# Optimization experiments

Hardware: AMD Instinct MI355X
Metric: run time of the kernel (lower is better)

The kernel has to match this reference:

```python
import jax, jax.numpy as jnp
import numpy as np

B, S, D = 2, 2048, 2048
H = 16
Q_LORA, KV_LORA = 1536, 512
ROPE_DIM, NOPE_DIM, V_DIM = 64, 64, 128
Q_HEAD_DIM = NOPE_DIM + ROPE_DIM  # 128
ROPE_THETA, ROPE_RATIO = 10000.0, 1.0


def setup_inputs() -> dict:
    key = jax.random.key(0)
    ks = jax.random.split(key, 6)
    std = 0.02
    return {
        "hidden_states": jax.random.normal(ks[0], (B, S, D), jnp.float32),
        "Wqa": jax.random.normal(ks[1], (D, Q_LORA), jnp.float32) * std,
        "Wqb": jax.random.normal(ks[2], (Q_LORA, H * Q_HEAD_DIM), jnp.float32) * std,
        "Wkva": jax.random.normal(ks[3], (D, KV_LORA + ROPE_DIM), jnp.float32) * std,
        "Wkvb": jax.random.normal(ks[4], (KV_LORA, H * (NOPE_DIM + V_DIM)), jnp.float32) * std,
        "Wo": jax.random.normal(ks[5], (H * V_DIM, D), jnp.float32) * std,
    }


def _rope_tables(seq_len):
    half = ROPE_DIM // 2
    inv_freq = ROPE_RATIO / (ROPE_THETA ** (jnp.arange(half, dtype=jnp.float32) * 2.0 / ROPE_DIM))
    freqs = jnp.arange(seq_len, dtype=jnp.float32)[:, None] * inv_freq[None, :]  # [S, half]
    return jnp.cos(freqs), jnp.sin(freqs)


def _apply_rope(x, cos, sin):
    # interleaved even/odd rotation, matches torch stack+flatten
    x_even = x[..., 0::2]
    x_odd = x[..., 1::2]
    r_even = x_even * cos - x_odd * sin
    r_odd = x_odd * cos + x_even * sin
    return jnp.stack([r_even, r_odd], axis=-1).reshape(x.shape)


def reference(hidden_states, Wqa, Wqb, Wkva, Wkvb, Wo):
    b, s, _ = hidden_states.shape
    scale = Q_HEAD_DIM ** -0.5

    # query compression path
    q_latent = hidden_states @ Wqa                             # [B,S,Q_LORA]
    q = (q_latent @ Wqb).reshape(b, s, H, Q_HEAD_DIM)
    q = jnp.transpose(q, (0, 2, 1, 3))                          # [B,H,S,q_head_dim]
    q_nope, q_pe = q[..., :NOPE_DIM], q[..., NOPE_DIM:]

    # kv compression
    kv_comp = hidden_states @ Wkva                              # [B,S,KV_LORA+ROPE]
    c_kv, k_pe = kv_comp[..., :KV_LORA], kv_comp[..., KV_LORA:]

    cos, sin = _rope_tables(s)                                  # [S, ROPE_DIM//2]
    q_pe = _apply_rope(q_pe, cos, sin)                          # [B,H,S,ROPE]
    k_pe = _apply_rope(k_pe, cos, sin)                          # [B,S,ROPE]

    # kv decompression
    kv = (c_kv @ Wkvb).reshape(b, s, H, NOPE_DIM + V_DIM)
    kv = jnp.transpose(kv, (0, 2, 1, 3))                        # [B,H,S,nope+v]
    k_nope, v = kv[..., :NOPE_DIM], kv[..., NOPE_DIM:]

    k_pe_b = jnp.broadcast_to(k_pe[:, None], (b, H, s, ROPE_DIM))
    q_full = jnp.concatenate([q_nope, q_pe], axis=-1)           # [B,H,S,128]
    k_full = jnp.concatenate([k_nope, k_pe_b], axis=-1)         # [B,H,S,128]

    scores = jnp.einsum('bhqd,bhkd->bhqk', q_full, k_full) * scale
    causal = jnp.tril(jnp.ones((s, s), dtype=bool))
    scores = jnp.where(causal[None, None], scores, jnp.finfo(scores.dtype).min)
    probs = jax.nn.softmax(scores, axis=-1)
    attn = jnp.einsum('bhqk,bhkd->bhqd', probs, v)              # [B,H,S,V_DIM]

    out = jnp.transpose(attn, (0, 2, 1, 3)).reshape(b, s, H * V_DIM)
    return out @ Wo                                             # [B,S,D]
```

## Files before the change

kernel.cpp:

```cpp
#include <hip/hip_runtime.h>
#include <hip/hip_bf16.h>
#include <cstdint>
#include <cstddef>

typedef __bf16 bf16_t;
typedef __attribute__((ext_vector_type(4))) __bf16 bf16x4;
typedef __attribute__((ext_vector_type(8))) __bf16 bf16x8;
typedef __attribute__((ext_vector_type(4))) float f32x4;

#define S_ 2048
#define H_ 16
#define NTOK 4096

__device__ __forceinline__ f32x4 mfma16x16(bf16x8 a, bf16x8 b, f32x4 c) {
  return __builtin_amdgcn_mfma_f32_16x16x32_bf16(a, b, c, 0, 0, 0);
}
__device__ __forceinline__ bf16x8 load8(const bf16_t* p) {
  return *reinterpret_cast<const bf16x8*>(p);
}
__device__ __forceinline__ void load_lds16(const void* g, void* l) {
  __builtin_amdgcn_global_load_lds(
      (const __attribute__((address_space(1))) uint32_t*)g,
      (__attribute__((address_space(3))) uint32_t*)l, 16, 0, 0);
}


__global__ void cast_bf16_k(const float* __restrict__ in, bf16_t* __restrict__ out, int n) {
  int idx = blockIdx.x * 256 + threadIdx.x;
  int i4 = idx * 4;
  if (i4 >= n) return;
  float4 v = *reinterpret_cast<const float4*>(in + i4);
  out[i4 + 0] = (bf16_t)v.x;
  out[i4 + 1] = (bf16_t)v.y;
  out[i4 + 2] = (bf16_t)v.z;
  out[i4 + 3] = (bf16_t)v.w;
}

__global__ void rope_tables_k(float* __restrict__ cosT, float* __restrict__ sinT) {
  int idx = blockIdx.x * 256 + threadIdx.x;
  if (idx >= S_ * 32) return;
  int s = idx >> 5, i = idx & 31;
  float inv = powf(10000.0f, -(2.0f * (float)i) / 64.0f);
  float fr = (float)s * inv;
  cosT[idx] = cosf(fr);
  sinT[idx] = sinf(fr);
}

struct TDesc {
  const float* src;
  bf16_t* dst;
  int K, Nsrc, bxc, off, perm;
};
struct TDesc5 {
  TDesc d[5];
};

__global__ void transpose_cast_multi_k(TDesc5 ds) {
  __shared__ float tile[32][33];
  const int bid = blockIdx.x;
  int i = 0;
#pragma unroll
  for (int j = 1; j < 5; ++j)
    if (bid >= ds.d[j].off) i = j;
  const float* __restrict__ in = ds.d[i].src;
  bf16_t* __restrict__ out = ds.d[i].dst;
  const int K = ds.d[i].K, Nsrc = ds.d[i].Nsrc;
  const int local = bid - ds.d[i].off;
  const int n0 = (local % ds.d[i].bxc) * 32;
  const int k0 = (local / ds.d[i].bxc) * 32;
  int srcn0 = n0;
  if (ds.d[i].perm) {
    srcn0 = (n0 < 1024) ? ((n0 >> 6) * 192 + (n0 & 63))
                        : (((n0 - 1024) >> 7) * 192 + 64 + ((n0 - 1024) & 127));
  }
  int tx = threadIdx.x & 31, ty = threadIdx.x >> 5;
#pragma unroll
  for (int r = 0; r < 4; ++r) {
    int k = k0 + ty + r * 8, n = srcn0 + tx;
    tile[ty + r * 8][tx] = (n < Nsrc) ? in[(size_t)k * Nsrc + n] : 0.0f;
  }
  __syncthreads();
#pragma unroll
  for (int r = 0; r < 4; ++r) {
    int n = n0 + ty + r * 8, k = k0 + tx;
    out[(size_t)n * K + k] = (bf16_t)tile[tx][ty + r * 8];
  }
}


__device__ __forceinline__ void gemm_loop64(const bf16_t* __restrict__ A, int lda,
                                            const bf16_t* __restrict__ Bt, int K, int m0, int n0,
                                            int tid, bf16_t* Al, bf16_t* Bl, f32x4 (&acc)[4][4]) {
  const int wid = tid >> 6, lane = tid & 63;
  const int wm = (wid >> 1) * 64, wn = (wid & 1) * 64;
  const int srow8 = lane >> 3, c8 = lane & 7;
  const int swz8 = c8 ^ srow8;
  const int lr = lane & 15, lg = lane >> 4;
  const int e = lr & 7;

  const bf16_t* ag = A + (size_t)(m0 + wid * 32 + srow8) * lda + (swz8 << 3);
  const bf16_t* bg = Bt + (size_t)(n0 + wid * 32 + srow8) * K + (swz8 << 3);

  auto STAGE = [&](int buf, int k0) {
    bf16_t* ab = Al + buf * (128 * 64);
    bf16_t* bb = Bl + buf * (128 * 64);
#pragma unroll
    for (int rr = 0; rr < 4; ++rr) {
      load_lds16(ag + (size_t)(rr * 8) * lda + k0, &ab[(wid * 32 + rr * 8) * 64]);
      load_lds16(bg + (size_t)(rr * 8) * K + k0, &bb[(wid * 32 + rr * 8) * 64]);
    }
  };

  STAGE(0, 0);
  int cur = 0;
  for (int k0 = 0; k0 < K; k0 += 64) {
    if (k0 + 64 < K) {
      STAGE(cur ^ 1, k0 + 64);
      __builtin_amdgcn_sched_barrier(0);
      asm volatile("s_waitcnt vmcnt(8)" ::: "memory");
    } else {
      asm volatile("s_waitcnt vmcnt(0)" ::: "memory");
    }
    __builtin_amdgcn_sched_barrier(0);
    __builtin_amdgcn_s_barrier();
    __builtin_amdgcn_sched_barrier(0);
    const bf16_t* Ab = Al + cur * (128 * 64);
    const bf16_t* Bb = Bl + cur * (128 * 64);
#pragma unroll
    for (int kk = 0; kk < 2; ++kk) {
      bf16x8 af[4], bfr[4];
#pragma unroll
      for (int i = 0; i < 4; ++i) {
        af[i] = load8(&Ab[(wm + i * 16 + lr) * 64 + (((kk * 4 + lg) ^ e) << 3)]);
        bfr[i] = load8(&Bb[(wn + i * 16 + lr) * 64 + (((kk * 4 + lg) ^ e) << 3)]);
      }
#pragma unroll
      for (int i = 0; i < 4; ++i)
#pragma unroll
        for (int j = 0; j < 4; ++j) acc[i][j] = mfma16x16(af[i], bfr[j], acc[i][j]);
    }
    __builtin_amdgcn_sched_barrier(0);
    __builtin_amdgcn_s_barrier();
    cur ^= 1;
  }
}


__global__ __launch_bounds__(256) void gemm_lat_k(const bf16_t* __restrict__ A,
                                                  const bf16_t* __restrict__ Bt,
                                                  bf16_t* __restrict__ C,
                                                  const float* __restrict__ cosT,
                                                  const float* __restrict__ sinT) {
  __shared__ alignas(16) bf16_t Al[2 * 128 * 64];
  __shared__ alignas(16) bf16_t Bl[2 * 128 * 64];
  const int tid = threadIdx.x;
  const int sw = (blockIdx.x & 7) * 68 + (blockIdx.x >> 3);
  const int m0 = (sw / 17) * 128, n0 = (sw % 17) * 128;
  f32x4 acc[4][4] = {};
  gemm_loop64(A, 2048, Bt, 2048, m0, n0, tid, Al, Bl, acc);

  const int wid = tid >> 6, lane = tid & 63;
  const int wm = (wid >> 1) * 64, wn = (wid & 1) * 64;
  const int lr = lane & 15, lg = lane >> 4;
  const bool rope = (n0 == 2048) && (wn == 0);
  const int ir_base = lr >> 1;
  const bool odd = lane & 1;
#pragma unroll
  for (int i = 0; i < 4; ++i)
#pragma unroll
    for (int j = 0; j < 4; ++j) {
      float v4[4];
#pragma unroll
      for (int r = 0; r < 4; ++r) v4[r] = acc[i][j][r];
      if (rope) {
        const int ir = j * 8 + ir_base;
#pragma unroll
        for (int r = 0; r < 4; ++r) {
          const int srow_ = (m0 + wm + i * 16 + lg * 4 + r) & (S_ - 1);
          float c = cosT[srow_ * 32 + ir], sn = sinT[srow_ * 32 + ir];
          float partner = __shfl_xor(v4[r], 1);
          v4[r] = odd ? (v4[r] * c + partner * sn) : (v4[r] * c - partner * sn);
        }
      }
#pragma unroll
      for (int r = 0; r < 4; ++r) {
        int row = m0 + wm + i * 16 + lg * 4 + r;
        int col = n0 + wn + j * 16 + lr;
        C[(size_t)row * 2176 + col] = (bf16_t)v4[r];
      }
    }
}


__global__ __launch_bounds__(256) void gemm_qkv_k(const bf16_t* __restrict__ lat,
                                                  const bf16_t* __restrict__ Wqbt,
                                                  const bf16_t* __restrict__ Wkvbt,
                                                  bf16_t* __restrict__ qb,
                                                  bf16_t* __restrict__ knb,
                                                  bf16_t* __restrict__ vT,
                                                  const float* __restrict__ cosT,
                                                  const float* __restrict__ sinT, float qscale) {
  __shared__ alignas(16) bf16_t Al[2 * 128 * 64];
  __shared__ alignas(16) bf16_t Bl[2 * 128 * 64];
  const int tid = threadIdx.x;
  const int sw = (blockIdx.x & 7) * 160 + (blockIdx.x >> 3);
  const int wid = tid >> 6, lane = tid & 63;
  const int wm = (wid >> 1) * 64, wn = (wid & 1) * 64;
  const int lr = lane & 15, lg = lane >> 4;
  f32x4 acc[4][4] = {};
  const int r5 = sw % 5, q5 = sw / 5;

  if (r5 < 2) {
    const int qi = q5 * 2 + r5;
    const int m0 = (qi >> 4) * 128, n0 = (qi & 15) * 128;
    gemm_loop64(lat, 2176, Wqbt, 1536, m0, n0, tid, Al, Bl, acc);
    const bool rope = (wn == 64);
    const int ir_base = lr >> 1;
    const bool odd = lane & 1;
#pragma unroll
    for (int i = 0; i < 4; ++i)
#pragma unroll
      for (int j = 0; j < 4; ++j) {
        float v4[4];
#pragma unroll
        for (int r = 0; r < 4; ++r) v4[r] = acc[i][j][r] * qscale;
        if (rope) {
          const int ir = j * 8 + ir_base;
#pragma unroll
          for (int r = 0; r < 4; ++r) {
            const int srow_ = (m0 + wm + i * 16 + lg * 4 + r) & (S_ - 1);
            float c = cosT[srow_ * 32 + ir], sn = sinT[srow_ * 32 + ir];
            float partner = __shfl_xor(v4[r], 1);
            v4[r] = odd ? (v4[r] * c + partner * sn) : (v4[r] * c - partner * sn);
          }
        }
#pragma unroll
        for (int r = 0; r < 4; ++r) {
          int row = m0 + wm + i * 16 + lg * 4 + r;
          int col = n0 + wn + j * 16 + lr;
          qb[(size_t)row * 2048 + col] = (bf16_t)v4[r];
        }
      }
  } else {
    const int ki = q5 * 3 + (r5 - 2);
    const int m0 = (ki / 24) * 128, n0 = (ki % 24) * 128;
    gemm_loop64(lat + 1536, 2176, Wkvbt, 512, m0, n0, tid, Al, Bl, acc);
    if (n0 < 1024) {
#pragma unroll
      for (int i = 0; i < 4; ++i)
#pragma unroll
        for (int j = 0; j < 4; ++j)
#pragma unroll
          for (int r = 0; r < 4; ++r) {
            int row = m0 + wm + i * 16 + lg * 4 + r;
            int col = n0 + wn + j * 16 + lr;
            knb[(size_t)row * 1024 + col] = (bf16_t)acc[i][j][r];
          }
    } else {
#pragma unroll
      for (int i = 0; i < 4; ++i) {
        const int row0 = m0 + wm + i * 16 + lg * 4;
        const int bb = row0 >> 11;
        const int s0 = row0 & (S_ - 1);
#pragma unroll
        for (int j = 0; j < 4; ++j) {
          const int idx = n0 + wn + j * 16 + lr - 1024;
          const int h = idx >> 7, d = idx & 127;
          bf16x4 pk;
#pragma unroll
          for (int r = 0; r < 4; ++r) pk[r] = (bf16_t)acc[i][j][r];
          *reinterpret_cast<bf16x4*>(&vT[((size_t)(bb * 16 + h) * 128 + d) * 2048 + s0]) = pk;
        }
      }
    }
  }
}


__global__ __launch_bounds__(256) void gemm_out_k(const bf16_t* __restrict__ A,
                                                  const bf16_t* __restrict__ Bt,
                                                  float* __restrict__ C) {
  __shared__ alignas(16) bf16_t Al[2 * 128 * 64];
  __shared__ alignas(16) bf16_t Bl[2 * 128 * 64];
  const int tid = threadIdx.x;
  const int sw = (blockIdx.x & 7) * 64 + (blockIdx.x >> 3);
  const int m0 = (sw >> 4) * 128, n0 = (sw & 15) * 128;
  f32x4 acc[4][4] = {};
  gemm_loop64(A, 2048, Bt, 2048, m0, n0, tid, Al, Bl, acc);
  const int wid = tid >> 6, lane = tid & 63;
  const int wm = (wid >> 1) * 64, wn = (wid & 1) * 64;
  const int lr = lane & 15, lg = lane >> 4;
#pragma unroll
  for (int i = 0; i < 4; ++i)
#pragma unroll
    for (int j = 0; j < 4; ++j)
#pragma unroll
      for (int r = 0; r < 4; ++r) {
        int row = m0 + wm + i * 16 + lg * 4 + r;
        int col = n0 + wn + j * 16 + lr;
        C[(size_t)row * 2048 + col] = acc[i][j][r];
      }
}

__global__ __launch_bounds__(256) void attn_fused(const bf16_t* __restrict__ q,
                                                  const bf16_t* __restrict__ knb,
                                                  const bf16_t* __restrict__ lat,
                                                  const bf16_t* __restrict__ vT,
                                                  bf16_t* __restrict__ out) {
  __shared__ alignas(16) bf16_t Kn[64 * 64];
  __shared__ alignas(16) bf16_t Kp[64 * 64];
  __shared__ alignas(16) bf16_t Vt[128 * 64];
  __shared__ alignas(16) bf16_t Pl[4][16 * 64];
  const int tid = threadIdx.x, wid = tid >> 6, lane = tid & 63;
  const int bid = blockIdx.x;
  const int g = bid >> 8;
  const int x = (bid >> 5) & 7;
  const int bh = bid & 31;
  const int qt = (g & 1) ? (24 - g * 8 + x) : (31 - g * 8 - x);
  const int b = bh >> 4, h = bh & 15;
  const int tokb = b * S_;
  const int lr = lane & 15, lg = lane >> 4;
  const int srow8 = lane >> 3, c8 = lane & 7;
  const int swz8 = c8 ^ srow8;
  bf16_t* Pw = &Pl[wid][0];

  bf16x8 ones;
#pragma unroll
  for (int j = 0; j < 8; ++j) ones[j] = (bf16_t)1.0f;

  bf16x8 qf[4];
  {
    const int qrow = qt * 64 + wid * 16 + lr;
    const bf16_t* qp = q + (size_t)(tokb + qrow) * 2048 + h * 128 + lg * 8;
#pragma unroll
    for (int ds = 0; ds < 4; ++ds) qf[ds] = load8(qp + ds * 32);
  }

  f32x4 o[8] = {};
  f32x4 o8 = {};
  float m = -1e30f;
  const int qr_glob = qt * 64 + wid * 16 + lr;

  for (int t = 0; t <= qt; ++t) {
    const int kb = t * 64;
#pragma unroll
    for (int rr = 0; rr < 2; ++rr) {
      const int r0 = wid * 16 + rr * 8;
      const size_t tk = (size_t)(tokb + kb + r0 + srow8);
      load_lds16(knb + tk * 1024 + h * 64 + (swz8 << 3), &Kn[r0 * 64]);
      load_lds16(lat + tk * 2176 + 2048 + (swz8 << 3), &Kp[r0 * 64]);
    }
#pragma unroll
    for (int rr = 0; rr < 4; ++rr) {
      const int r0 = wid * 32 + rr * 8;
      load_lds16(vT + ((size_t)bh * 128 + r0 + srow8) * 2048 + kb + (swz8 << 3), &Vt[r0 * 64]);
    }
    __syncthreads();

    f32x4 s[4];
    __builtin_amdgcn_s_setprio(1);
#pragma unroll
    for (int kt = 0; kt < 4; ++kt) {
      const int row = kt * 16 + lr;
      const int e = lr & 7;
      bf16x8 kf0 = load8(&Kn[row * 64 + ((lg ^ e) << 3)]);
      bf16x8 kf1 = load8(&Kn[row * 64 + (((lg + 4) ^ e) << 3)]);
      bf16x8 kf2 = load8(&Kp[row * 64 + ((lg ^ e) << 3)]);
      bf16x8 kf3 = load8(&Kp[row * 64 + (((lg + 4) ^ e) << 3)]);
      f32x4 acc = {0.f, 0.f, 0.f, 0.f};
      acc = mfma16x16(kf0, qf[0], acc);
      acc = mfma16x16(kf1, qf[1], acc);
      acc = mfma16x16(kf2, qf[2], acc);
      acc = mfma16x16(kf3, qf[3], acc);
      s[kt] = acc;
    }
    __builtin_amdgcn_s_setprio(0);

    if (t == qt) {
#pragma unroll
      for (int kt = 0; kt < 4; ++kt)
#pragma unroll
        for (int r = 0; r < 4; ++r) {
          const int key = kb + kt * 16 + lg * 4 + r;
          if (key > qr_glob) s[kt][r] = -1e30f;
        }
    }

    float tm;
    {
      float a0 = fmaxf(fmaxf(s[0][0], s[0][1]), fmaxf(s[0][2], s[0][3]));
      float a1 = fmaxf(fmaxf(s[1][0], s[1][1]), fmaxf(s[1][2], s[1][3]));
      float a2 = fmaxf(fmaxf(s[2][0], s[2][1]), fmaxf(s[2][2], s[2][3]));
      float a3 = fmaxf(fmaxf(s[3][0], s[3][1]), fmaxf(s[3][2], s[3][3]));
      tm = fmaxf(fmaxf(a0, a1), fmaxf(a2, a3));
      tm = fmaxf(tm, __shfl_xor(tm, 16));
      tm = fmaxf(tm, __shfl_xor(tm, 32));
    }
    if (!__all(tm - m <= 8.0f)) {
      float mn = fmaxf(m, tm);
      float corr = exp2f(m - mn);
      m = mn;
      float corrv[4];
#pragma unroll
      for (int r = 0; r < 4; ++r) corrv[r] = __shfl(corr, lg * 4 + r);
#pragma unroll
      for (int r = 0; r < 4; ++r) {
        o8[r] *= corrv[r];
#pragma unroll
        for (int n = 0; n < 8; ++n) o[n][r] *= corrv[r];
      }
    }
#pragma unroll
    for (int kt = 0; kt < 4; ++kt)
#pragma unroll
      for (int r = 0; r < 4; ++r) s[kt][r] = exp2f(s[kt][r] - m);

#pragma unroll
    for (int kt = 0; kt < 4; ++kt) {
      bf16x4 pk;
#pragma unroll
      for (int r = 0; r < 4; ++r) pk[r] = (bf16_t)s[kt][r];
      const int c = kt * 2 + (lg >> 1);
      *reinterpret_cast<bf16x4*>(&Pw[lr * 64 + ((c ^ (lr & 7)) << 3) + ((lg & 1) << 2)]) = pk;
    }

    __builtin_amdgcn_s_setprio(1);
#pragma unroll
    for (int ks = 0; ks < 2; ++ks) {
      const int e = lr & 7;
      bf16x8 pa = load8(&Pw[lr * 64 + (((ks * 4 + lg) ^ e) << 3)]);
#pragma unroll
      for (int n = 0; n < 8; ++n) {
        bf16x8 vb = load8(&Vt[(n * 16 + lr) * 64 + (((ks * 4 + lg) ^ e) << 3)]);
        o[n] = mfma16x16(pa, vb, o[n]);
      }
      o8 = mfma16x16(pa, ones, o8);
    }
    __builtin_amdgcn_s_setprio(0);
    __syncthreads();
  }

  float linv[4];
#pragma unroll
  for (int r = 0; r < 4; ++r) linv[r] = __builtin_amdgcn_rcpf(o8[r]);
#pragma unroll
  for (int n = 0; n < 8; ++n)
#pragma unroll
    for (int r = 0; r < 4; ++r) {
      const int qr = qt * 64 + wid * 16 + lg * 4 + r;
      out[(size_t)(tokb + qr) * 2048 + h * 128 + n * 16 + lr] = (bf16_t)(o[n][r] * linv[r]);
    }
}


extern "C" void kernel_launch(void* const* d_in, const int* in_sizes, int n_in, void* d_out,
                              int out_size, void* d_ws, size_t ws_size, hipStream_t stream) {
  const float* hs = (const float*)d_in[0];
  const float* Wqa = (const float*)d_in[1];
  const float* Wqb = (const float*)d_in[2];
  const float* Wkva = (const float*)d_in[3];
  const float* Wkvb = (const float*)d_in[4];
  const float* Wo = (const float*)d_in[5];
  float* out = (float*)d_out;

  char* ws = (char*)d_ws;
  size_t off = 0;
  auto alloc = [&](size_t bytes) {
    void* p = ws + off;
    off += (bytes + 255) & ~(size_t)255;
    return p;
  };
  bf16_t* hsb = (bf16_t*)alloc((size_t)NTOK * 2048 * 2);
  bf16_t* W1t = (bf16_t*)alloc((size_t)2176 * 2048 * 2);
  bf16_t* Wqbt = (bf16_t*)alloc((size_t)2048 * 1536 * 2);
  bf16_t* Wkvbt = (bf16_t*)alloc((size_t)3072 * 512 * 2);
  bf16_t* Wot = (bf16_t*)alloc((size_t)2048 * 2048 * 2);
  bf16_t* lat = (bf16_t*)alloc((size_t)NTOK * 2176 * 2);
  bf16_t* qb = (bf16_t*)alloc((size_t)NTOK * 2048 * 2);
  bf16_t* knb = (bf16_t*)alloc((size_t)NTOK * 1024 * 2);
  bf16_t* attn = (bf16_t*)alloc((size_t)NTOK * 2048 * 2);
  bf16_t* vT = (bf16_t*)alloc((size_t)32 * 128 * 2048 * 2);
  float* cosT = (float*)alloc((size_t)S_ * 32 * 4);
  float* sinT = (float*)alloc((size_t)S_ * 32 * 4);

  cast_bf16_k<<<(NTOK * 2048 / 4 + 255) / 256, 256, 0, stream>>>(hs, hsb, NTOK * 2048);
  rope_tables_k<<<(S_ * 32 + 255) / 256, 256, 0, stream>>>(cosT, sinT);
  {
    TDesc5 ds;
    int o0 = 0;
    auto add = [&](int i, const float* src, bf16_t* dst, int K, int Nsrc, int Nout, int perm) {
      int bxc = Nout / 32, cnt = bxc * (K / 32);
      ds.d[i] = TDesc{src, dst, K, Nsrc, bxc, o0, perm};
      o0 += cnt;
    };
    add(0, Wqa, W1t, 2048, 1536, 1536, 0);
    add(1, Wkva, W1t + (size_t)1536 * 2048, 2048, 576, 640, 0);
    add(2, Wqb, Wqbt, 1536, 2048, 2048, 0);
    add(3, Wkvb, Wkvbt, 512, 3072, 3072, 1);
    add(4, Wo, Wot, 2048, 2048, 2048, 0);
    transpose_cast_multi_k<<<o0, 256, 0, stream>>>(ds);
  }

  gemm_lat_k<<<dim3(544), 256, 0, stream>>>(hsb, W1t, lat, cosT, sinT);
  const float scale = 0.08838834764831845f * 1.4426950408889634f;
  gemm_qkv_k<<<dim3(1280), 256, 0, stream>>>(lat, Wqbt, Wkvbt, qb, knb, vT, cosT, sinT, scale);
  attn_fused<<<dim3(1024), 256, 0, stream>>>(qb, knb, lat, vT, attn);
  gemm_out_k<<<dim3(512), 256, 0, stream>>>(attn, Wot, out);
}
```

Baseline: 275.3 us.

## Double-buffer K/V tiles in attention to overlap global-to-LDS loads with compute

Splits the K-nope, K-rope and V-transpose LDS tiles into two buffers and issues the load of tile t+1 before computing on tile t. A manual vmcnt wait and s_barrier replace the per-iteration __syncthreads so the prefetch stays in flight during the MFMA work. LDS use rises from about 40 KB to 72 KB per block, which may lower occupancy, and the hand-written waitcnt count has to match the number of loads issued per stage.

```diff
diff --git a/kernel.cpp b/kernel.cpp
--- a/kernel.cpp
+++ b/kernel.cpp
@@ -307,9 +307,9 @@
                                                   const bf16_t* __restrict__ lat,
                                                   const bf16_t* __restrict__ vT,
                                                   bf16_t* __restrict__ out) {
-  __shared__ alignas(16) bf16_t Kn[64 * 64];
-  __shared__ alignas(16) bf16_t Kp[64 * 64];
-  __shared__ alignas(16) bf16_t Vt[128 * 64];
+  __shared__ alignas(16) bf16_t Kn[2][64 * 64];
+  __shared__ alignas(16) bf16_t Kp[2][64 * 64];
+  __shared__ alignas(16) bf16_t Vt[2][128 * 64];
   __shared__ alignas(16) bf16_t Pl[4][16 * 64];
   const int tid = threadIdx.x, wid = tid >> 6, lane = tid & 63;
   const int bid = blockIdx.x;
@@ -341,21 +341,36 @@
   float m = -1e30f;
   const int qr_glob = qt * 64 + wid * 16 + lr;
 
-  for (int t = 0; t <= qt; ++t) {
+  auto STAGE = [&](int buf, int t) {
     const int kb = t * 64;
 #pragma unroll
     for (int rr = 0; rr < 2; ++rr) {
       const int r0 = wid * 16 + rr * 8;
       const size_t tk = (size_t)(tokb + kb + r0 + srow8);
-      load_lds16(knb + tk * 1024 + h * 64 + (swz8 << 3), &Kn[r0 * 64]);
-      load_lds16(lat + tk * 2176 + 2048 + (swz8 << 3), &Kp[r0 * 64]);
+      load_lds16(knb + tk * 1024 + h * 64 + (swz8 << 3), &Kn[buf][r0 * 64]);
+      load_lds16(lat + tk * 2176 + 2048 + (swz8 << 3), &Kp[buf][r0 * 64]);
     }
 #pragma unroll
     for (int rr = 0; rr < 4; ++rr) {
       const int r0 = wid * 32 + rr * 8;
-      load_lds16(vT + ((size_t)bh * 128 + r0 + srow8) * 2048 + kb + (swz8 << 3), &Vt[r0 * 64]);
-    }
-    __syncthreads();
+      load_lds16(vT + ((size_t)bh * 128 + r0 + srow8) * 2048 + kb + (swz8 << 3),
+                 &Vt[buf][r0 * 64]);
+    }
+  };
+
+  STAGE(0, 0);
+  for (int t = 0; t <= qt; ++t) {
+    const int cur = t & 1;
+    if (t < qt) {
+      STAGE(cur ^ 1, t + 1);
+      __builtin_amdgcn_sched_barrier(0);
+      asm volatile("s_waitcnt vmcnt(8)" ::: "memory");
+    } else {
+      asm volatile("s_waitcnt vmcnt(0)" ::: "memory");
+    }
+    __builtin_amdgcn_sched_barrier(0);
+    __builtin_amdgcn_s_barrier();
+    __builtin_amdgcn_sched_barrier(0);
 
     f32x4 s[4];
     __builtin_amdgcn_s_setprio(1);
@@ -363,10 +378,10 @@
     for (int kt = 0; kt < 4; ++kt) {
       const int row = kt * 16 + lr;
       const int e = lr & 7;
-      bf16x8 kf0 = load8(&Kn[row * 64 + ((lg ^ e) << 3)]);
-      bf16x8 kf1 = load8(&Kn[row * 64 + (((lg + 4) ^ e) << 3)]);
-      bf16x8 kf2 = load8(&Kp[row * 64 + ((lg ^ e) << 3)]);
-      bf16x8 kf3 = load8(&Kp[row * 64 + (((lg + 4) ^ e) << 3)]);
+      bf16x8 kf0 = load8(&Kn[cur][row * 64 + ((lg ^ e) << 3)]);
+      bf16x8 kf1 = load8(&Kn[cur][row * 64 + (((lg + 4) ^ e) << 3)]);
+      bf16x8 kf2 = load8(&Kp[cur][row * 64 + ((lg ^ e) << 3)]);
+      bf16x8 kf3 = load8(&Kp[cur][row * 64 + (((lg + 4) ^ e) << 3)]);
       f32x4 acc = {0.f, 0.f, 0.f, 0.f};
       acc = mfma16x16(kf0, qf[0], acc);
       acc = mfma16x16(kf1, qf[1], acc);
@@ -377,6 +392,7 @@
     __builtin_amdgcn_s_setprio(0);
 
     if (t == qt) {
+      const int kb = t * 64;
 #pragma unroll
       for (int kt = 0; kt < 4; ++kt)
 #pragma unroll
@@ -431,13 +447,14 @@
       bf16x8 pa = load8(&Pw[lr * 64 + (((ks * 4 + lg) ^ e) << 3)]);
 #pragma unroll
       for (int n = 0; n < 8; ++n) {
-        bf16x8 vb = load8(&Vt[(n * 16 + lr) * 64 + (((ks * 4 + lg) ^ e) << 3)]);
+        bf16x8 vb = load8(&Vt[cur][(n * 16 + lr) * 64 + (((ks * 4 + lg) ^ e) << 3)]);
         o[n] = mfma16x16(pa, vb, o[n]);
       }
       o8 = mfma16x16(pa, ones, o8);
     }
     __builtin_amdgcn_s_setprio(0);
-    __syncthreads();
+    __builtin_amdgcn_sched_barrier(0);
+    __builtin_amdgcn_s_barrier();
   }
 
   float linv[4];
```

Result: no change. 277.2 us (+0.7%).

## Switch attention to 32x32x16 MFMA with two waves per block

Applied to the files above, without the earlier changes.

Rewrites the fused attention kernel to use 32x32x16 bf16 MFMA instructions, with each of two waves handling 32 query rows instead of four waves with 16 rows each. Blocks shrink to 128 threads and each wave loads more of the K/V tiles into LDS. The goal is better MFMA efficiency and fewer LDS fragment reads per FLOP. In exchange, per-wave register pressure rises from the larger accumulators, and there are fewer waves per block to hide latency.

```diff
diff --git a/kernel.cpp b/kernel.cpp
--- a/kernel.cpp
+++ b/kernel.cpp
@@ -7,6 +7,7 @@
 typedef __attribute__((ext_vector_type(4))) __bf16 bf16x4;
 typedef __attribute__((ext_vector_type(8))) __bf16 bf16x8;
 typedef __attribute__((ext_vector_type(4))) float f32x4;
+typedef __attribute__((ext_vector_type(16))) float f32x16;
 
 #define S_ 2048
 #define H_ 16
@@ -14,6 +15,9 @@
 
 __device__ __forceinline__ f32x4 mfma16x16(bf16x8 a, bf16x8 b, f32x4 c) {
   return __builtin_amdgcn_mfma_f32_16x16x32_bf16(a, b, c, 0, 0, 0);
+}
+__device__ __forceinline__ f32x16 mfma32(bf16x8 a, bf16x8 b, f32x16 c) {
+  return __builtin_amdgcn_mfma_f32_32x32x16_bf16(a, b, c, 0, 0, 0);
 }
 __device__ __forceinline__ bf16x8 load8(const bf16_t* p) {
   return *reinterpret_cast<const bf16x8*>(p);
@@ -302,7 +306,7 @@
       }
 }
 
-__global__ __launch_bounds__(256) void attn_fused(const bf16_t* __restrict__ q,
+__global__ __launch_bounds__(128) void attn_fused(const bf16_t* __restrict__ q,
                                                   const bf16_t* __restrict__ knb,
                                                   const bf16_t* __restrict__ lat,
                                                   const bf16_t* __restrict__ vT,
@@ -310,8 +314,8 @@
   __shared__ alignas(16) bf16_t Kn[64 * 64];
   __shared__ alignas(16) bf16_t Kp[64 * 64];
   __shared__ alignas(16) bf16_t Vt[128 * 64];
-  __shared__ alignas(16) bf16_t Pl[4][16 * 64];
-  const int tid = threadIdx.x, wid = tid >> 6, lane = tid & 63;
+  __shared__ alignas(16) bf16_t Pl[2][32 * 64];
+  const int tid = threadIdx.x, wv = tid >> 6, lane = tid & 63;
   const int bid = blockIdx.x;
   const int g = bid >> 8;
   const int x = (bid >> 5) & 7;
@@ -319,136 +323,135 @@
   const int qt = (g & 1) ? (24 - g * 8 + x) : (31 - g * 8 - x);
   const int b = bh >> 4, h = bh & 15;
   const int tokb = b * S_;
-  const int lr = lane & 15, lg = lane >> 4;
+  const int l31 = lane & 31, hi = lane >> 5;
+  const int e7 = l31 & 7;
   const int srow8 = lane >> 3, c8 = lane & 7;
   const int swz8 = c8 ^ srow8;
-  bf16_t* Pw = &Pl[wid][0];
+  bf16_t* Pw = &Pl[wv][0];
 
   bf16x8 ones;
 #pragma unroll
   for (int j = 0; j < 8; ++j) ones[j] = (bf16_t)1.0f;
 
-  bf16x8 qf[4];
+  const int qrow = qt * 64 + wv * 32 + l31;
+  bf16x8 qf[8];
   {
-    const int qrow = qt * 64 + wid * 16 + lr;
-    const bf16_t* qp = q + (size_t)(tokb + qrow) * 2048 + h * 128 + lg * 8;
-#pragma unroll
-    for (int ds = 0; ds < 4; ++ds) qf[ds] = load8(qp + ds * 32);
-  }
-
-  f32x4 o[8] = {};
-  f32x4 o8 = {};
+    const bf16_t* qp = q + (size_t)(tokb + qrow) * 2048 + h * 128 + hi * 8;
+#pragma unroll
+    for (int grp = 0; grp < 8; ++grp) qf[grp] = load8(qp + grp * 16);
+  }
+
+  f32x16 o[4] = {};
+  f32x16 o8 = {};
   float m = -1e30f;
-  const int qr_glob = qt * 64 + wid * 16 + lr;
 
   for (int t = 0; t <= qt; ++t) {
     const int kb = t * 64;
 #pragma unroll
-    for (int rr = 0; rr < 2; ++rr) {
-      const int r0 = wid * 16 + rr * 8;
+    for (int rr = 0; rr < 4; ++rr) {
+      const int r0 = wv * 32 + rr * 8;
       const size_t tk = (size_t)(tokb + kb + r0 + srow8);
       load_lds16(knb + tk * 1024 + h * 64 + (swz8 << 3), &Kn[r0 * 64]);
       load_lds16(lat + tk * 2176 + 2048 + (swz8 << 3), &Kp[r0 * 64]);
     }
 #pragma unroll
-    for (int rr = 0; rr < 4; ++rr) {
-      const int r0 = wid * 32 + rr * 8;
+    for (int rr = 0; rr < 8; ++rr) {
+      const int r0 = wv * 64 + rr * 8;
       load_lds16(vT + ((size_t)bh * 128 + r0 + srow8) * 2048 + kb + (swz8 << 3), &Vt[r0 * 64]);
     }
     __syncthreads();
 
-    f32x4 s[4];
+    f32x16 sv[2];
     __builtin_amdgcn_s_setprio(1);
 #pragma unroll
-    for (int kt = 0; kt < 4; ++kt) {
-      const int row = kt * 16 + lr;
-      const int e = lr & 7;
-      bf16x8 kf0 = load8(&Kn[row * 64 + ((lg ^ e) << 3)]);
-      bf16x8 kf1 = load8(&Kn[row * 64 + (((lg + 4) ^ e) << 3)]);
-      bf16x8 kf2 = load8(&Kp[row * 64 + ((lg ^ e) << 3)]);
-      bf16x8 kf3 = load8(&Kp[row * 64 + (((lg + 4) ^ e) << 3)]);
-      f32x4 acc = {0.f, 0.f, 0.f, 0.f};
-      acc = mfma16x16(kf0, qf[0], acc);
-      acc = mfma16x16(kf1, qf[1], acc);
-      acc = mfma16x16(kf2, qf[2], acc);
-      acc = mfma16x16(kf3, qf[3], acc);
-      s[kt] = acc;
+    for (int kb32 = 0; kb32 < 2; ++kb32) {
+      const int krow = kb32 * 32 + l31;
+      const int ke7 = krow & 7;
+      f32x16 acc = {};
+#pragma unroll
+      for (int ds = 0; ds < 4; ++ds) {
+        bf16x8 kf = load8(&Kn[krow * 64 + (((ds * 2 + hi) ^ ke7) << 3)]);
+        acc = mfma32(kf, qf[ds], acc);
+      }
+#pragma unroll
+      for (int ds = 0; ds < 4; ++ds) {
+        bf16x8 kf = load8(&Kp[krow * 64 + (((ds * 2 + hi) ^ ke7) << 3)]);
+        acc = mfma32(kf, qf[4 + ds], acc);
+      }
+      sv[kb32] = acc;
     }
     __builtin_amdgcn_s_setprio(0);
 
     if (t == qt) {
 #pragma unroll
-      for (int kt = 0; kt < 4; ++kt)
-#pragma unroll
-        for (int r = 0; r < 4; ++r) {
-          const int key = kb + kt * 16 + lg * 4 + r;
-          if (key > qr_glob) s[kt][r] = -1e30f;
+      for (int kb32 = 0; kb32 < 2; ++kb32)
+#pragma unroll
+        for (int r = 0; r < 16; ++r) {
+          const int key = kb + kb32 * 32 + (r & 3) + 8 * (r >> 2) + 4 * hi;
+          if (key > qrow) sv[kb32][r] = -1e30f;
         }
     }
 
-    float tm;
-    {
-      float a0 = fmaxf(fmaxf(s[0][0], s[0][1]), fmaxf(s[0][2], s[0][3]));
-      float a1 = fmaxf(fmaxf(s[1][0], s[1][1]), fmaxf(s[1][2], s[1][3]));
-      float a2 = fmaxf(fmaxf(s[2][0], s[2][1]), fmaxf(s[2][2], s[2][3]));
-      float a3 = fmaxf(fmaxf(s[3][0], s[3][1]), fmaxf(s[3][2], s[3][3]));
-      tm = fmaxf(fmaxf(a0, a1), fmaxf(a2, a3));
-      tm = fmaxf(tm, __shfl_xor(tm, 16));
-      tm = fmaxf(tm, __shfl_xor(tm, 32));
-    }
+    float tm = sv[0][0];
+#pragma unroll
+    for (int r = 1; r < 16; ++r) tm = fmaxf(tm, sv[0][r]);
+#pragma unroll
+    for (int r = 0; r < 16; ++r) tm = fmaxf(tm, sv[1][r]);
+    tm = fmaxf(tm, __shfl_xor(tm, 32));
+
     if (!__all(tm - m <= 8.0f)) {
       float mn = fmaxf(m, tm);
       float corr = exp2f(m - mn);
       m = mn;
-      float corrv[4];
-#pragma unroll
-      for (int r = 0; r < 4; ++r) corrv[r] = __shfl(corr, lg * 4 + r);
-#pragma unroll
-      for (int r = 0; r < 4; ++r) {
-        o8[r] *= corrv[r];
-#pragma unroll
-        for (int n = 0; n < 8; ++n) o[n][r] *= corrv[r];
-      }
-    }
-#pragma unroll
-    for (int kt = 0; kt < 4; ++kt)
-#pragma unroll
-      for (int r = 0; r < 4; ++r) s[kt][r] = exp2f(s[kt][r] - m);
-
-#pragma unroll
-    for (int kt = 0; kt < 4; ++kt) {
-      bf16x4 pk;
-#pragma unroll
-      for (int r = 0; r < 4; ++r) pk[r] = (bf16_t)s[kt][r];
-      const int c = kt * 2 + (lg >> 1);
-      *reinterpret_cast<bf16x4*>(&Pw[lr * 64 + ((c ^ (lr & 7)) << 3) + ((lg & 1) << 2)]) = pk;
-    }
+#pragma unroll
+      for (int r = 0; r < 16; ++r) {
+        float cv = __shfl(corr, (r & 3) + 8 * (r >> 2) + 4 * hi);
+        o8[r] *= cv;
+#pragma unroll
+        for (int db = 0; db < 4; ++db) o[db][r] *= cv;
+      }
+    }
+#pragma unroll
+    for (int kb32 = 0; kb32 < 2; ++kb32)
+#pragma unroll
+      for (int r = 0; r < 16; ++r) sv[kb32][r] = exp2f(sv[kb32][r] - m);
+
+#pragma unroll
+    for (int kb32 = 0; kb32 < 2; ++kb32)
+#pragma unroll
+      for (int i = 0; i < 4; ++i) {
+        bf16x4 pk;
+#pragma unroll
+        for (int r = 0; r < 4; ++r) pk[r] = (bf16_t)sv[kb32][i * 4 + r];
+        const int c = kb32 * 4 + i;
+        *reinterpret_cast<bf16x4*>(&Pw[l31 * 64 + ((c ^ e7) << 3) + (hi << 2)]) = pk;
+      }
 
     __builtin_amdgcn_s_setprio(1);
 #pragma unroll
-    for (int ks = 0; ks < 2; ++ks) {
-      const int e = lr & 7;
-      bf16x8 pa = load8(&Pw[lr * 64 + (((ks * 4 + lg) ^ e) << 3)]);
-#pragma unroll
-      for (int n = 0; n < 8; ++n) {
-        bf16x8 vb = load8(&Vt[(n * 16 + lr) * 64 + (((ks * 4 + lg) ^ e) << 3)]);
-        o[n] = mfma16x16(pa, vb, o[n]);
-      }
-      o8 = mfma16x16(pa, ones, o8);
+    for (int ks = 0; ks < 4; ++ks) {
+      bf16x8 pa = load8(&Pw[l31 * 64 + (((ks * 2 + hi) ^ e7) << 3)]);
+#pragma unroll
+      for (int db = 0; db < 4; ++db) {
+        const int vrow = db * 32 + l31;
+        bf16x8 vb = load8(&Vt[vrow * 64 + (((ks * 2 + hi) ^ (vrow & 7)) << 3)]);
+        o[db] = mfma32(pa, vb, o[db]);
+      }
+      o8 = mfma32(pa, ones, o8);
     }
     __builtin_amdgcn_s_setprio(0);
     __syncthreads();
   }
 
-  float linv[4];
-#pragma unroll
-  for (int r = 0; r < 4; ++r) linv[r] = __builtin_amdgcn_rcpf(o8[r]);
-#pragma unroll
-  for (int n = 0; n < 8; ++n)
-#pragma unroll
-    for (int r = 0; r < 4; ++r) {
-      const int qr = qt * 64 + wid * 16 + lg * 4 + r;
-      out[(size_t)(tokb + qr) * 2048 + h * 128 + n * 16 + lr] = (bf16_t)(o[n][r] * linv[r]);
+  float linv[16];
+#pragma unroll
+  for (int r = 0; r < 16; ++r) linv[r] = __builtin_amdgcn_rcpf(o8[r]);
+#pragma unroll
+  for (int db = 0; db < 4; ++db)
+#pragma unroll
+    for (int r = 0; r < 16; ++r) {
+      const int row = qt * 64 + wv * 32 + (r & 3) + 8 * (r >> 2) + 4 * hi;
+      out[(size_t)(tokb + row) * 2048 + h * 128 + db * 32 + l31] = (bf16_t)(o[db][r] * linv[r]);
     }
 }
 
@@ -504,6 +507,6 @@
   gemm_lat_k<<<dim3(544), 256, 0, stream>>>(hsb, W1t, lat, cosT, sinT);
   const float scale = 0.08838834764831845f * 1.4426950408889634f;
   gemm_qkv_k<<<dim3(1280), 256, 0, stream>>>(lat, Wqbt, Wkvbt, qb, knb, vT, cosT, sinT, scale);
-  attn_fused<<<dim3(1024), 256, 0, stream>>>(qb, knb, lat, vT, attn);
+  attn_fused<<<dim3(1024), 128, 0, stream>>>(qb, knb, lat, vT, attn);
   gemm_out_k<<<dim3(512), 256, 0, stream>>>(attn, Wot, out);
 }
```

Measured after the change: 295.6 us. 1.07x slower.
